# Kernel optimization log

Hardware: AMD Instinct MI355X
Metric: run time of the kernel (lower is better)

## Reference

```python
import jax, jax.numpy as jnp
import numpy as np

N_REFLNS = 4_194_304
N_DIM = 64
N_IMAGES = 1024


def setup_inputs() -> dict:
    key = jax.random.key(0)
    kx, kid = jax.random.split(key)
    x = jax.random.normal(kx, (N_REFLNS, N_DIM), dtype=jnp.float32)
    image_id = jnp.sort(jax.random.randint(kid, (N_REFLNS,), 0, N_IMAGES, dtype=jnp.int32))
    return {"x": x, "image_id": image_id, "n_images": N_IMAGES}


def reference(x, image_id, n_images):
    # torch.unique(return_inverse, return_counts) over ids 0..n_images-1 with all
    # ids present: unique ids == arange(n_images), inverse indices == image_id.
    counts = jax.ops.segment_sum(
        jnp.ones_like(image_id), image_id, num_segments=n_images
    )  # [n_images] int
    sums = jax.ops.segment_sum(x, image_id, num_segments=n_images)  # [n_images, n_dim]
    # guard against an (astronomically unlikely) empty segment
    denom = jnp.maximum(counts, 1).astype(x.dtype)[:, None]
    averaged = sums / denom
    return averaged, image_id, counts
```

## Files before the change

kernel.cpp:

```cpp
#include <hip/hip_runtime.h>

#define N_DIM       64
#define N_IMAGES    1024
#define ROWS_PER_BLOCK 4096
#define THREADS     256

__global__ __launch_bounds__(THREADS) void ImageAverage_phaseA(
    const float* __restrict__ x,
    const int*   __restrict__ ids,
    float*       __restrict__ accum,
    int*         __restrict__ counts,
    float*       __restrict__ out_id)
{
    const int t = threadIdx.x;
    const long long blockRow0 = (long long)blockIdx.x * ROWS_PER_BLOCK;

    {
        const int4* idv  = (const int4*)(ids + blockRow0);
        float4*     outv = (float4*)(out_id + blockRow0);
        const int niter = ROWS_PER_BLOCK / 4 / THREADS;
        #pragma unroll
        for (int k = 0; k < niter; ++k) {
            int4 v = idv[k * THREADS + t];
            outv[k * THREADS + t] =
                make_float4((float)v.x, (float)v.y, (float)v.z, (float)v.w);
        }
    }

    const int dimGroup = t & 15;
    const int d0       = dimGroup * 4;
    const int rowOff   = t >> 4;
    const bool isCounter = (dimGroup == 0);

    float4 sum = make_float4(0.f, 0.f, 0.f, 0.f);
    int    cnt = 0;

    long long row = blockRow0 + rowOff;
    int cur = ids[row];

    #pragma unroll 4
    for (int it = 0; it < ROWS_PER_BLOCK / 16; ++it, row += 16) {
        const int id = ids[row];
        if (id != cur) {
            float* a = accum + (long long)cur * N_DIM + d0;
            atomicAdd(a + 0, sum.x);
            atomicAdd(a + 1, sum.y);
            atomicAdd(a + 2, sum.z);
            atomicAdd(a + 3, sum.w);
            if (isCounter) atomicAdd(&counts[cur], cnt);
            sum = make_float4(0.f, 0.f, 0.f, 0.f);
            cnt = 0;
            cur = id;
        }
        const float4 v = *(const float4*)(x + row * N_DIM + d0);
        sum.x += v.x; sum.y += v.y; sum.z += v.z; sum.w += v.w;
        cnt++;
    }
    {
        float* a = accum + (long long)cur * N_DIM + d0;
        atomicAdd(a + 0, sum.x);
        atomicAdd(a + 1, sum.y);
        atomicAdd(a + 2, sum.z);
        atomicAdd(a + 3, sum.w);
        if (isCounter) atomicAdd(&counts[cur], cnt);
    }
}

__global__ __launch_bounds__(THREADS) void ImageAverage_phaseB(
    const float* __restrict__ accum,
    const int*   __restrict__ counts,
    float*       __restrict__ out_avg,
    float*       __restrict__ out_counts)
{
    const int i = blockIdx.x * blockDim.x + threadIdx.x;
    if (i < N_IMAGES * N_DIM) {
        const int img = i >> 6;
        const int c = counts[img];
        const float denom = (float)(c > 0 ? c : 1);
        out_avg[i] = accum[i] / denom;
    }
    if (i < N_IMAGES) {
        out_counts[i] = (float)counts[i];
    }
}

extern "C" void kernel_launch(void* const* d_in, const int* in_sizes, int n_in,
                              void* d_out, int out_size, void* d_ws, size_t ws_size,
                              hipStream_t stream) {
    const float* x   = (const float*)d_in[0];
    const int*   ids = (const int*)d_in[1];
    const int n_reflns = in_sizes[1];

    float* out_avg    = (float*)d_out;
    float* out_id     = out_avg + (size_t)N_IMAGES * N_DIM;
    float* out_counts = out_id + (size_t)n_reflns;

    float* accum  = (float*)d_ws;
    int*   counts = (int*)((char*)d_ws + (size_t)N_IMAGES * N_DIM * sizeof(float));

    hipMemsetAsync(d_ws, 0,
                   (size_t)N_IMAGES * N_DIM * sizeof(float) + (size_t)N_IMAGES * sizeof(int),
                   stream);

    const int gridA = n_reflns / ROWS_PER_BLOCK;
    ImageAverage_phaseA<<<gridA, THREADS, 0, stream>>>(x, ids, accum, counts, out_id);

    const int nB = N_IMAGES * N_DIM;
    ImageAverage_phaseB<<<(nB + THREADS - 1) / THREADS, THREADS, 0, stream>>>(
        accum, counts, out_avg, out_counts);
}
```

Before: 1.363 ms.

## Add sorted-id fast path with nontemporal loads and halve rows per block

```diff
diff --git a/kernel.cpp b/kernel.cpp
--- a/kernel.cpp
+++ b/kernel.cpp
@@ -1,9 +1,12 @@
 #include <hip/hip_runtime.h>
 
-#define N_DIM       64
-#define N_IMAGES    1024
-#define ROWS_PER_BLOCK 4096
-#define THREADS     256
+#define N_DIM          64
+#define N_IMAGES       1024
+#define ROWS_PER_BLOCK 2048
+#define THREADS        256
+
+typedef float v4f __attribute__((ext_vector_type(4)));
+typedef int   v4i __attribute__((ext_vector_type(4)));
 
 __global__ __launch_bounds__(THREADS) void ImageAverage_phaseA(
     const float* __restrict__ x,
@@ -16,14 +19,15 @@
     const long long blockRow0 = (long long)blockIdx.x * ROWS_PER_BLOCK;
 
     {
-        const int4* idv  = (const int4*)(ids + blockRow0);
-        float4*     outv = (float4*)(out_id + blockRow0);
+        const v4i* idv  = (const v4i*)(ids + blockRow0);
+        v4f*       outv = (v4f*)(out_id + blockRow0);
         const int niter = ROWS_PER_BLOCK / 4 / THREADS;
         #pragma unroll
         for (int k = 0; k < niter; ++k) {
-            int4 v = idv[k * THREADS + t];
-            outv[k * THREADS + t] =
-                make_float4((float)v.x, (float)v.y, (float)v.z, (float)v.w);
+            v4i v = idv[k * THREADS + t];
+            v4f f;
+            f.x = (float)v.x; f.y = (float)v.y; f.z = (float)v.z; f.w = (float)v.w;
+            __builtin_nontemporal_store(f, &outv[k * THREADS + t]);
         }
     }
 
@@ -32,29 +36,43 @@
     const int rowOff   = t >> 4;
     const bool isCounter = (dimGroup == 0);
 
-    float4 sum = make_float4(0.f, 0.f, 0.f, 0.f);
-    int    cnt = 0;
+    v4f sum = {0.f, 0.f, 0.f, 0.f};
+    int cnt = 0;
 
     long long row = blockRow0 + rowOff;
     int cur = ids[row];
 
-    #pragma unroll 4
-    for (int it = 0; it < ROWS_PER_BLOCK / 16; ++it, row += 16) {
-        const int id = ids[row];
-        if (id != cur) {
-            float* a = accum + (long long)cur * N_DIM + d0;
-            atomicAdd(a + 0, sum.x);
-            atomicAdd(a + 1, sum.y);
-            atomicAdd(a + 2, sum.z);
-            atomicAdd(a + 3, sum.w);
-            if (isCounter) atomicAdd(&counts[cur], cnt);
-            sum = make_float4(0.f, 0.f, 0.f, 0.f);
-            cnt = 0;
-            cur = id;
+    const int NGROUPS = ROWS_PER_BLOCK / 16 / 4;
+    for (int g = 0; g < NGROUPS; ++g, row += 64) {
+        const int idLast = ids[row + 48];
+        if (idLast == cur) {
+            const v4f a = __builtin_nontemporal_load((const v4f*)(x + (row     ) * N_DIM + d0));
+            const v4f b = __builtin_nontemporal_load((const v4f*)(x + (row + 16) * N_DIM + d0));
+            const v4f c = __builtin_nontemporal_load((const v4f*)(x + (row + 32) * N_DIM + d0));
+            const v4f d = __builtin_nontemporal_load((const v4f*)(x + (row + 48) * N_DIM + d0));
+            sum += (a + b) + (c + d);
+            cnt += 4;
+        } else {
+            #pragma unroll
+            for (int k = 0; k < 4; ++k) {
+                const long long r = row + 16 * k;
+                const int id = ids[r];
+                if (id != cur) {
+                    float* a = accum + (long long)cur * N_DIM + d0;
+                    atomicAdd(a + 0, sum.x);
+                    atomicAdd(a + 1, sum.y);
+                    atomicAdd(a + 2, sum.z);
+                    atomicAdd(a + 3, sum.w);
+                    if (isCounter) atomicAdd(&counts[cur], cnt);
+                    sum = (v4f){0.f, 0.f, 0.f, 0.f};
+                    cnt = 0;
+                    cur = id;
+                }
+                const v4f v = __builtin_nontemporal_load((const v4f*)(x + r * N_DIM + d0));
+                sum += v;
+                cnt++;
+            }
         }
-        const float4 v = *(const float4*)(x + row * N_DIM + d0);
-        sum.x += v.x; sum.y += v.y; sum.z += v.z; sum.w += v.w;
-        cnt++;
     }
     {
         float* a = accum + (long long)cur * N_DIM + d0;
```

Result: faster. 1.330 ms (-2.5%).
